# Optimization experiments

Measured on AMD Instinct MI355X. Metric: run time of the kernel, lower is better.

Reference implementation:

```python
import jax, jax.numpy as jnp
import numpy as np

OUT_SIZE = 14
CUTOFF = 0.2
VAR0 = 4            # var[0], mixin_factor = 0.0 -> current std = var[0]
BETA = 4.0
N_SQ = OUT_SIZE * OUT_SIZE
TAU = 0.5 / N_SQ
BATCH = 256
CHANNELS = 512


def _gkern_np(kernlen, std, vmin, vmax):
    n = np.arange(kernlen) - (kernlen - 1) / 2.0
    w = np.exp(-(n ** 2) / (2.0 * std * std))
    g = np.outer(w, w)
    return g * (vmax - vmin) + vmin


def _build_templates():
    n = OUT_SIZE
    base = _gkern_np(2 * n - 1, VAR0, -CUTOFF, 1.0)
    base = np.maximum(base, 0.0) * 2.0 - 1.0
    base = TAU * np.clip(BETA * base / n, -1.0, None)  # clamp(min=-1) only
    # unfold(0,n,1).unfold(1,n,1).reshape(-1,n,n) == sliding windows, row-major
    t = np.lib.stride_tricks.sliding_window_view(base, (n, n)).reshape(-1, n, n)
    t = np.flip(t, axis=0).copy()  # torch.flip(templates, dims=(0,))
    templates_f = jnp.asarray(t, jnp.float32)                    # (n^2, n, n)
    neg = -TAU * jnp.ones((1, n, n), jnp.float32)
    templates_b = jnp.concatenate([templates_f, neg], axis=0)    # (n^2+1, n, n)
    alpha = N_SQ / (1.0 + N_SQ)
    p_T = jnp.asarray(
        np.array([alpha / N_SQ] * N_SQ + [1.0 - alpha], np.float32))  # (n^2+1,)
    return templates_f, templates_b, p_T


def setup_inputs() -> dict:
    key = jax.random.key(0)
    templates_f, templates_b, p_T = _build_templates()
    x = jax.random.normal(key, (BATCH, CHANNELS, OUT_SIZE, OUT_SIZE), jnp.float32)
    return {"x": x, "templates_f": templates_f,
            "templates_b": templates_b, "p_T": p_T}


def reference(x, templates_f, templates_b, p_T):
    B, C, H, W = x.shape
    tau = 0.5 / (H * W)
    # max_pool2d with kernel == full spatial extent -> flat argmax per (b, c)
    idx = jnp.argmax(x.reshape(B, C, H * W), axis=-1)            # (B, C) int
    sel = templates_f[idx]                                       # (B, C, H, W)
    mask = sel / jnp.max(sel)                                    # global max
    mask = jax.nn.relu(mask - CUTOFF) / CUTOFF
    x_masked = x * mask
    # local loss (mutual-information style) on the masked activations
    tr_x_T = jnp.einsum('bcwh,twh->cbt', x_masked * tau, templates_b)  # (C,B,T)
    p_x_T = jax.nn.softmax(tr_x_T, axis=1)                       # softmax over b
    p_x = jnp.einsum('t,cbt->cb', p_T, p_x_T)                    # (C, B)
    log_ratio = jnp.log(p_x_T / p_x[:, :, None])                 # (C, B, T)
    p_x_T_log = jnp.einsum('cbt,cbt->ct', p_x_T, log_ratio)      # (C, T)
    loss = -jnp.einsum('t,ct->c', p_T, p_x_T_log)                # (C,)
    return x_masked, mask, loss
```

## Files before the change

### kernel.cpp

```cpp
#include <hip/hip_runtime.h>

#define BB 256
#define CCH 512
#define HW 196
#define TT 197
#define TROWS 208
#define NFRAG (13 * 7)
#define ASHORTS (NFRAG * 64 * 8)
#define CST (CCH * TROWS)
#define QMAX_SHORTS (4 * 7 * 512)

typedef __attribute__((ext_vector_type(8))) short bf16x8;
typedef __attribute__((ext_vector_type(4))) float f32x4;
typedef __attribute__((ext_vector_type(4))) unsigned short us4;

__device__ __forceinline__ unsigned short f2bf(float f) {
    union { float f; unsigned u; } v; v.f = f;
    unsigned r = v.u + 0x7FFFu + ((v.u >> 16) & 1u);
    return (unsigned short)(r >> 16);
}
__device__ __forceinline__ float bf2f(unsigned short h) {
    union { unsigned u; float f; } v; v.u = ((unsigned)h) << 16;
    return v.f;
}

__global__ void prep(const float* __restrict__ tf, const float* __restrict__ tb,
                     const float* __restrict__ pT,
                     float* __restrict__ wsf, unsigned short* __restrict__ tb_bf,
                     float* __restrict__ pT_pad) {
    if (blockIdx.x < 182) {
        int i = blockIdx.x * 256 + threadIdx.x;
        int frag = i >> 9;
        int s    = i & 511;
        int mt = frag / 7, kt = frag % 7;
        int lane = s >> 3, j = s & 7;
        int r = mt * 16 + (lane & 15);
        int k = kt * 32 + (lane >> 4) * 8 + j;
        const float tau = 0.5f / 196.0f;
        float v = (r < TT && k < HW) ? tb[r * HW + k] * tau : 0.0f;
        tb_bf[i] = f2bf(v);
    } else {
        if (threadIdx.x < TROWS)
            pT_pad[threadIdx.x] = (threadIdx.x < TT) ? pT[threadIdx.x] : 0.0f;
        __shared__ float red[256];
        float m = -1e30f;
        for (int i = threadIdx.x; i < HW * HW; i += 256) m = fmaxf(m, tf[i]);
        red[threadIdx.x] = m;
        __syncthreads();
        for (int s = 128; s > 0; s >>= 1) {
            if (threadIdx.x < s) red[threadIdx.x] = fmaxf(red[threadIdx.x], red[threadIdx.x + s]);
            __syncthreads();
        }
        if (threadIdx.x == 0) wsf[0] = red[0];
    }
}

extern "C" __global__ __launch_bounds__(256)
__attribute__((amdgpu_waves_per_eu(4, 4)))
void k1_main(const float* __restrict__ x, const float* __restrict__ tf,
             const unsigned short* __restrict__ tb_bf, const float* __restrict__ wsf,
             float* __restrict__ xm_out, float* __restrict__ mask_out,
             float* __restrict__ colp, unsigned short* __restrict__ trs)
{
    __shared__ unsigned short Alds[QMAX_SHORTS];
    __shared__ float s_col[4][TROWS];

    const int tid  = threadIdx.x;
    const int lane = tid & 63;
    const int w    = tid >> 6;
    const int l15  = lane & 15, lg = lane >> 4;
    const int c    = blockIdx.x >> 2, g = blockIdx.x & 3;
    const float rg = 1.0f / wsf[0];

    {
        const f32x4* src = (const f32x4*)tb_bf;
        f32x4* dst = (f32x4*)Alds;
        #pragma unroll
        for (int it = 0; it < 7; ++it) dst[tid + it * 256] = src[tid + it * 256];
    }

    const int b = g * 64 + w * 16 + l15;
    const size_t rowoff = ((size_t)b * CCH + c) * HW;
    const float* xrow = x + rowoff;

    f32x4 u[13];
    #pragma unroll
    for (int kt = 0; kt < 6; ++kt) {
        u[2 * kt]     = *(const f32x4*)(xrow + kt * 32 + lg * 8);
        u[2 * kt + 1] = *(const f32x4*)(xrow + kt * 32 + lg * 8 + 4);
    }
    if (lg == 0) u[12] = *(const f32x4*)(xrow + 192);
    else         u[12] = (f32x4){-__builtin_inff(), -__builtin_inff(),
                                 -__builtin_inff(), -__builtin_inff()};

    float bv = -__builtin_inff(); int bi = 0;
    #pragma unroll
    for (int j = 0; j < 13; ++j) {
        const int k0 = (j < 12) ? (((j >> 1) * 8 + lg * 2 + (j & 1)) * 4) : 192;
        #pragma unroll
        for (int e = 0; e < 4; ++e) {
            float v = u[j][e];
            if (v > bv) { bv = v; bi = k0 + e; }
        }
    }
    #pragma unroll
    for (int m = 16; m <= 32; m <<= 1) {
        float ov = __shfl_xor(bv, m, 64);
        int   oi = __shfl_xor(bi, m, 64);
        if (ov > bv || (ov == bv && oi < bi)) { bv = ov; bi = oi; }
    }

    const float* selrow = tf + (size_t)bi * HW;
    float* xmrow = xm_out + rowoff;
    float* mkrow = mask_out + rowoff;
    bf16x8 fr[7];

    #pragma unroll
    for (int kt = 0; kt < 6; ++kt) {
        #pragma unroll
        for (int h = 0; h < 2; ++h) {
            const int k0 = kt * 32 + lg * 8 + h * 4;
            f32x4 sel = *(const f32x4*)(selrow + k0);
            f32x4 mk, xm;
            #pragma unroll
            for (int e = 0; e < 4; ++e) {
                float m = fmaxf(sel[e] * rg - 0.2f, 0.0f) * 5.0f;
                mk[e] = m;
                xm[e] = u[2 * kt + h][e] * m;
            }
            *(f32x4*)(xmrow + k0) = xm;
            *(f32x4*)(mkrow + k0) = mk;
            #pragma unroll
            for (int e = 0; e < 4; ++e) fr[kt][h * 4 + e] = (short)f2bf(xm[e]);
        }
    }
    {
        fr[6] = (bf16x8){0, 0, 0, 0, 0, 0, 0, 0};
        if (lg == 0) {
            f32x4 sel = *(const f32x4*)(selrow + 192);
            f32x4 mk, xm;
            #pragma unroll
            for (int e = 0; e < 4; ++e) {
                float m = fmaxf(sel[e] * rg - 0.2f, 0.0f) * 5.0f;
                mk[e] = m;
                xm[e] = u[12][e] * m;
            }
            *(f32x4*)(xmrow + 192) = xm;
            *(f32x4*)(mkrow + 192) = mk;
            #pragma unroll
            for (int e = 0; e < 4; ++e) fr[6][e] = (short)f2bf(xm[e]);
        }
    }

    f32x4 acc[13];
    #pragma unroll
    for (int mt = 0; mt < 13; ++mt) acc[mt] = (f32x4){0.f, 0.f, 0.f, 0.f};

    const unsigned short* Abase = Alds + lane * 8;

    __syncthreads();
    #pragma unroll
    for (int mt = 0; mt < 4; ++mt) {
        #pragma unroll
        for (int kt = 0; kt < 7; ++kt)
            acc[mt] = __builtin_amdgcn_mfma_f32_16x16x32_bf16(
                *(const bf16x8*)(Abase + (mt * 7 + kt) * 512), fr[kt], acc[mt], 0, 0, 0);
    }
    __syncthreads();

    #pragma unroll
    for (int q = 1; q < 4; ++q) {
        const int m0 = 4 + (q - 1) * 3;
        {
            const f32x4* src = (const f32x4*)tb_bf + m0 * 7 * 64;
            f32x4* dst = (f32x4*)Alds;
            #pragma unroll
            for (int it = 0; it < 6; ++it) {
                int idx = tid + it * 256;
                if (idx < 1344) dst[idx] = src[idx];
            }
        }
        __syncthreads();
        #pragma unroll
        for (int mi = 0; mi < 3; ++mi) {
            const int mt = m0 + mi;
            #pragma unroll
            for (int kt = 0; kt < 7; ++kt)
                acc[mt] = __builtin_amdgcn_mfma_f32_16x16x32_bf16(
                    *(const bf16x8*)(Abase + (mi * 7 + kt) * 512), fr[kt], acc[mt], 0, 0, 0);
        }
        __syncthreads();
    }

    unsigned short* trow = trs + (((size_t)c * 4 + g) * 64 + w * 16 + l15) * TROWS;
    #pragma unroll
    for (int mt = 0; mt < 13; ++mt) {
        us4 pk;
        #pragma unroll
        for (int e = 0; e < 4; ++e) pk[e] = f2bf(acc[mt][e]);
        *(us4*)(trow + mt * 16 + lg * 4) = pk;

        f32x4 s;
        #pragma unroll
        for (int e = 0; e < 4; ++e) s[e] = __expf(acc[mt][e]);
        #pragma unroll
        for (int m = 1; m <= 8; m <<= 1) {
            #pragma unroll
            for (int e = 0; e < 4; ++e) s[e] += __shfl_xor(s[e], m, 64);
        }
        if (l15 == 0) *(f32x4*)(&s_col[w][mt * 16 + lg * 4]) = s;
    }
    __syncthreads();
    if (tid < TROWS) {
        float s = s_col[0][tid] + s_col[1][tid] + s_col[2][tid] + s_col[3][tid];
        colp[(size_t)g * CST + c * TROWS + tid] = s;
    }
}

extern "C" __global__ __launch_bounds__(256)
void k2_loss(const unsigned short* __restrict__ trs, const float* __restrict__ pT_pad,
             const float* __restrict__ colp, float* __restrict__ loss_part)
{
    __shared__ float rAs[TROWS];
    __shared__ float lAs[TROWS];
    __shared__ float pTs[TROWS];
    __shared__ float red[4];

    const int tid  = threadIdx.x;
    const int lane = tid & 63;
    const int w    = tid >> 6;
    const int c    = blockIdx.x >> 2, g = blockIdx.x & 3;

    if (tid < TROWS) {
        const float* cpc = colp + (size_t)c * TROWS + tid;
        float A = cpc[0] + cpc[CST] + cpc[2 * CST] + cpc[3 * CST];
        rAs[tid] = 1.0f / A;
        lAs[tid] = __logf(A);
        pTs[tid] = pT_pad[tid];
    }
    __syncthreads();

    const int p4 = tid & 3;
    const unsigned short* trow = trs + (((size_t)c * 4 + g) * 64 + (tid >> 2)) * TROWS;

    float px = 0.f, S1 = 0.f;
    #pragma unroll
    for (int j = 0; j < 13; ++j) {
        const int t0 = (p4 + 4 * j) * 4;
        us4 tv = *(const us4*)(trow + t0);
        #pragma unroll
        for (int e = 0; e < 4; ++e) {
            const int t = t0 + e;
            float tr = bf2f(tv[e]);
            float p  = __expf(tr) * rAs[t];
            px += pTs[t] * p;
            S1 += pTs[t] * p * (tr - lAs[t]);
        }
    }
    px += __shfl_xor(px, 1, 64);
    px += __shfl_xor(px, 2, 64);
    S1 += __shfl_xor(S1, 1, 64);
    S1 += __shfl_xor(S1, 2, 64);
    float part = (p4 == 0) ? (S1 - px * __logf(px)) : 0.0f;
    #pragma unroll
    for (int off = 4; off <= 32; off <<= 1) part += __shfl_xor(part, off, 64);
    if (lane == 0) red[w] = part;
    __syncthreads();
    if (tid == 0) loss_part[(size_t)c * 4 + g] = red[0] + red[1] + red[2] + red[3];
}

__global__ void k3_fin(const float* __restrict__ lp, float* __restrict__ loss_out) {
    int c = blockIdx.x * 256 + threadIdx.x;
    if (c < CCH)
        loss_out[c] = -(lp[4 * c] + lp[4 * c + 1] + lp[4 * c + 2] + lp[4 * c + 3]);
}

#define H1FRAG (7 * 7)
#define H2FRAG (6 * 7)
#define H1SHORTS (H1FRAG * 512)
#define H2SHORTS (H2FRAG * 512)

extern "C" __global__ __launch_bounds__(1024)
void fused_fb(const float* __restrict__ x, const float* __restrict__ tf,
              const float* __restrict__ pT, const unsigned short* __restrict__ tb_bf,
              const float* __restrict__ wsf,
              float* __restrict__ xm_out, float* __restrict__ mask_out,
              float* __restrict__ loss_out)
{
    extern __shared__ char smem[];
    unsigned short* Alds = (unsigned short*)smem;
    float* s_part = (float*)(smem + H1SHORTS * 2);
    float* rAs    = s_part + 16 * TROWS;
    float* pTs    = rAs + TROWS;
    float* red    = pTs + TROWS;

    const int c    = blockIdx.x;
    const int tid  = threadIdx.x;
    const int lane = tid & 63;
    const int w    = tid >> 6;
    const int l15  = lane & 15, lg = lane >> 4;
    const float rg = 1.0f / wsf[0];

    {
        const f32x4* src = (const f32x4*)tb_bf;
        f32x4* dst = (f32x4*)Alds;
        #pragma unroll
        for (int it = 0; it < 4; ++it) {
            int idx = tid + it * 1024;
            if (idx < H1SHORTS / 8) dst[idx] = src[idx];
        }
    }
    if (tid < TROWS) pTs[tid] = (tid < TT) ? pT[tid] : 0.0f;

    const int b = w * 16 + l15;
    const size_t rowoff = ((size_t)b * CCH + c) * HW;
    const float* xrow = x + rowoff;

    f32x4 u[13];
    #pragma unroll
    for (int kt = 0; kt < 6; ++kt) {
        u[2 * kt]     = *(const f32x4*)(xrow + kt * 32 + lg * 8);
        u[2 * kt + 1] = *(const f32x4*)(xrow + kt * 32 + lg * 8 + 4);
    }
    if (lg == 0) u[12] = *(const f32x4*)(xrow + 192);
    else         u[12] = (f32x4){-__builtin_inff(), -__builtin_inff(),
                                 -__builtin_inff(), -__builtin_inff()};

    float bv = -__builtin_inff(); int bi = 0;
    #pragma unroll
    for (int j = 0; j < 13; ++j) {
        const int k0 = (j < 12) ? (((j >> 1) * 8 + lg * 2 + (j & 1)) * 4) : 192;
        #pragma unroll
        for (int e = 0; e < 4; ++e) {
            float v = u[j][e];
            if (v > bv) { bv = v; bi = k0 + e; }
        }
    }
    #pragma unroll
    for (int m = 16; m <= 32; m <<= 1) {
        float ov = __shfl_xor(bv, m, 64);
        int   oi = __shfl_xor(bi, m, 64);
        if (ov > bv || (ov == bv && oi < bi)) { bv = ov; bi = oi; }
    }

    const float* selrow = tf + (size_t)bi * HW;
    float* xmrow = xm_out + rowoff;
    float* mkrow = mask_out + rowoff;
    bf16x8 fr[7];

    #pragma unroll
    for (int kt = 0; kt < 6; ++kt) {
        #pragma unroll
        for (int h = 0; h < 2; ++h) {
            const int k0 = kt * 32 + lg * 8 + h * 4;
            f32x4 sel = *(const f32x4*)(selrow + k0);
            f32x4 mk, xm;
            #pragma unroll
            for (int e = 0; e < 4; ++e) {
                float m = fmaxf(sel[e] * rg - 0.2f, 0.0f) * 5.0f;
                mk[e] = m;
                xm[e] = u[2 * kt + h][e] * m;
            }
            *(f32x4*)(xmrow + k0) = xm;
            *(f32x4*)(mkrow + k0) = mk;
            #pragma unroll
            for (int e = 0; e < 4; ++e) fr[kt][h * 4 + e] = (short)f2bf(xm[e]);
        }
    }
    {
        fr[6] = (bf16x8){0, 0, 0, 0, 0, 0, 0, 0};
        if (lg == 0) {
            f32x4 sel = *(const f32x4*)(selrow + 192);
            f32x4 mk, xm;
            #pragma unroll
            for (int e = 0; e < 4; ++e) {
                float m = fmaxf(sel[e] * rg - 0.2f, 0.0f) * 5.0f;
                mk[e] = m;
                xm[e] = u[12][e] * m;
            }
            *(f32x4*)(xmrow + 192) = xm;
            *(f32x4*)(mkrow + 192) = mk;
            #pragma unroll
            for (int e = 0; e < 4; ++e) fr[6][e] = (short)f2bf(xm[e]);
        }
    }

    __syncthreads();

    f32x4 acc[13];
    #pragma unroll
    for (int mt = 0; mt < 13; ++mt) acc[mt] = (f32x4){0.f, 0.f, 0.f, 0.f};

    const unsigned short* Abase = Alds + lane * 8;
    #pragma unroll
    for (int kt = 0; kt < 7; ++kt) {
        const bf16x8 bfrag = fr[kt];
        #pragma unroll
        for (int mt = 0; mt < 7; ++mt)
            acc[mt] = __builtin_amdgcn_mfma_f32_16x16x32_bf16(
                *(const bf16x8*)(Abase + (mt * 7 + kt) * 512), bfrag, acc[mt], 0, 0, 0);
    }
    __syncthreads();
    {
        const f32x4* src = (const f32x4*)(tb_bf + H1SHORTS);
        f32x4* dst = (f32x4*)Alds;
        #pragma unroll
        for (int it = 0; it < 3; ++it) {
            int idx = tid + it * 1024;
            if (idx < H2SHORTS / 8) dst[idx] = src[idx];
        }
    }
    __syncthreads();
    #pragma unroll
    for (int kt = 0; kt < 7; ++kt) {
        const bf16x8 bfrag = fr[kt];
        #pragma unroll
        for (int mt = 7; mt < 13; ++mt)
            acc[mt] = __builtin_amdgcn_mfma_f32_16x16x32_bf16(
                *(const bf16x8*)(Abase + ((mt - 7) * 7 + kt) * 512), bfrag, acc[mt], 0, 0, 0);
    }

    float* sp = s_part + w * TROWS;
    #pragma unroll
    for (int mt = 0; mt < 13; ++mt) {
        #pragma unroll
        for (int e = 0; e < 4; ++e) acc[mt][e] = __expf(acc[mt][e]);
        f32x4 s = acc[mt];
        #pragma unroll
        for (int m = 1; m <= 8; m <<= 1) {
            #pragma unroll
            for (int e = 0; e < 4; ++e) s[e] += __shfl_xor(s[e], m, 64);
        }
        if (l15 == 0) *(f32x4*)(sp + mt * 16 + lg * 4) = s;
    }
    __syncthreads();
    if (tid < TROWS) {
        float s = 0.f;
        #pragma unroll
        for (int w2 = 0; w2 < 16; ++w2) s += s_part[w2 * TROWS + tid];
        rAs[tid] = 1.0f / s;
    }
    __syncthreads();

    float px = 0.f;
    #pragma unroll
    for (int mt = 0; mt < 13; ++mt) {
        const int t0 = mt * 16 + lg * 4;
        f32x4 ra = *(const f32x4*)(rAs + t0);
        f32x4 pt = *(const f32x4*)(pTs + t0);
        #pragma unroll
        for (int e = 0; e < 4; ++e) {
            float p = acc[mt][e] * ra[e];
            acc[mt][e] = p;
            px += pt[e] * p;
        }
    }
    px += __shfl_xor(px, 16, 64);
    px += __shfl_xor(px, 32, 64);
    const float rpx = 1.0f / px;

    float part = 0.f;
    #pragma unroll
    for (int mt = 0; mt < 13; ++mt) {
        const int t0 = mt * 16 + lg * 4;
        f32x4 pt = *(const f32x4*)(pTs + t0);
        #pragma unroll
        for (int e = 0; e < 4; ++e) {
            float p = acc[mt][e];
            part += pt[e] * p * __logf(p * rpx);
        }
    }
    #pragma unroll
    for (int off = 32; off >= 1; off >>= 1) part += __shfl_xor(part, off, 64);
    if (lane == 0) red[w] = part;
    __syncthreads();
    if (tid == 0) {
        float s = 0.f;
        #pragma unroll
        for (int w2 = 0; w2 < 16; ++w2) s += red[w2];
        loss_out[c] = -s;
    }
}

extern "C" void kernel_launch(void* const* d_in, const int* in_sizes, int n_in,
                              void* d_out, int out_size, void* d_ws, size_t ws_size,
                              hipStream_t stream) {
    const float* x  = (const float*)d_in[0];
    const float* tf = (const float*)d_in[1];
    const float* tb = (const float*)d_in[2];
    const float* pT = (const float*)d_in[3];

    const size_t NOUT = (size_t)BB * CCH * HW;
    float* xm_out = (float*)d_out;
    float* mk_out = xm_out + NOUT;
    float* ls_out = mk_out + NOUT;

    char* wsp = (char*)d_ws;
    float*          wsf    = (float*)wsp;
    unsigned short* tb_bf  = (unsigned short*)(wsp + 64);
    float*          pT_pad = (float*)(wsp + 93312);
    float*          colp   = (float*)(wsp + 94208);
    float*          lpart  = (float*)(wsp + 1798144);
    unsigned short* trs    = (unsigned short*)(wsp + 1806336);
    const bool big = ws_size >= (size_t)1806336 + 54525952;

    prep<<<183, 256, 0, stream>>>(tf, tb, pT, wsf, tb_bf, pT_pad);

    if (big) {
        k1_main<<<2048, 256, 0, stream>>>(x, tf, tb_bf, wsf, xm_out, mk_out, colp, trs);
        k2_loss<<<2048, 256, 0, stream>>>(trs, pT_pad, colp, lpart);
        k3_fin<<<2, 256, 0, stream>>>(lpart, ls_out);
    } else {
        const size_t SMEM = (size_t)H1SHORTS * 2 + 16 * TROWS * 4
                          + 2 * TROWS * 4 + 16 * 4;
        (void)hipFuncSetAttribute((const void*)fused_fb,
                                  hipFuncAttributeMaxDynamicSharedMemorySize, (int)SMEM);
        fused_fb<<<dim3(CCH), dim3(1024), SMEM, stream>>>(x, tf, pT, tb_bf, wsf,
                                                          xm_out, mk_out, ls_out);
    }
}
```

Measured before the change: 168.1 us.

## Split elementwise masking into contiguous role blocks within a heterogeneous mega kernel

Converts k1_main into a multi-role kernel. Two of every three blocks process 32 contiguous (b,c) rows through LDS, computing argmax, mask and x_masked with fully coalesced float4 loads and stores. The remaining blocks only run the bf16 MFMA GEMM and write the transposed logits. Previously each GEMM block also wrote the strided xm and mask rows, so the output traffic was poorly coalesced. The cost is that the GEMM blocks read x a second time, and the fallback path now re-reads xm_out in a separate GEMM+loss kernel.

```diff
diff --git a/kernel.cpp b/kernel.cpp
--- a/kernel.cpp
+++ b/kernel.cpp
@@ -5,10 +5,15 @@
 #define HW 196
 #define TT 197
 #define TROWS 208
-#define NFRAG (13 * 7)
-#define ASHORTS (NFRAG * 64 * 8)
 #define CST (CCH * TROWS)
 #define QMAX_SHORTS (4 * 7 * 512)
+#define RPW 32
+#define F4PW (RPW * 49)
+#define H1FRAG (7 * 7)
+#define H2FRAG (6 * 7)
+#define H1SHORTS (H1FRAG * 512)
+#define H2SHORTS (H2FRAG * 512)
+#define MEGA_SMEM 32000
 
 typedef __attribute__((ext_vector_type(8))) short bf16x8;
 typedef __attribute__((ext_vector_type(4))) float f32x4;
@@ -57,20 +62,99 @@
 
 extern "C" __global__ __launch_bounds__(256)
 __attribute__((amdgpu_waves_per_eu(4, 4)))
-void k1_main(const float* __restrict__ x, const float* __restrict__ tf,
-             const unsigned short* __restrict__ tb_bf, const float* __restrict__ wsf,
-             float* __restrict__ xm_out, float* __restrict__ mask_out,
-             float* __restrict__ colp, unsigned short* __restrict__ trs)
+void mega(const float* __restrict__ x, const float* __restrict__ tf,
+          const unsigned short* __restrict__ tb_bf, const float* __restrict__ wsf,
+          float* __restrict__ xm_out, float* __restrict__ mask_out,
+          float* __restrict__ colp, unsigned short* __restrict__ trs, int mode)
 {
-    __shared__ unsigned short Alds[QMAX_SHORTS];
-    __shared__ float s_col[4][TROWS];
-
-    const int tid  = threadIdx.x;
+    extern __shared__ char sh[];
+    const int bid = blockIdx.x;
+    const int tid = threadIdx.x;
+    const float rg = 1.0f / wsf[0];
+
+    int role, idx;
+    if (mode == 0) { role = 0; idx = bid; }
+    else if (bid % 3 == 2) { role = 1; idx = (bid - 2) / 3; }
+    else { role = 0; idx = bid - (bid + 1) / 3; }
+
+    if (role == 0) {
+        float* xs  = (float*)sh;
+        int*   biL = (int*)(sh + RPW * HW * 4);
+
+        const size_t base4 = (size_t)idx * F4PW;
+        const f32x4* x4 = (const f32x4*)x + base4;
+        f32x4* xs4 = (f32x4*)xs;
+
+        f32x4 u[7];
+        #pragma unroll
+        for (int k = 0; k < 6; ++k) u[k] = x4[tid + k * 256];
+        if (tid < F4PW - 1536) u[6] = x4[tid + 1536];
+        #pragma unroll
+        for (int k = 0; k < 6; ++k) xs4[tid + k * 256] = u[k];
+        if (tid < F4PW - 1536) xs4[tid + 1536] = u[6];
+        __syncthreads();
+
+        {
+            const int row = tid >> 3;
+            const int o   = tid & 7;
+            float bv = -__builtin_inff(); int bi = 0;
+            #pragma unroll
+            for (int t = 0; t < 7; ++t) {
+                const int j = o + 8 * t;
+                if (j < 49) {
+                    f32x4 xv = xs4[row * 49 + j];
+                    const int k0 = j * 4;
+                    #pragma unroll
+                    for (int e = 0; e < 4; ++e) {
+                        float v = xv[e];
+                        if (v > bv) { bv = v; bi = k0 + e; }
+                    }
+                }
+            }
+            #pragma unroll
+            for (int m = 1; m <= 4; m <<= 1) {
+                float ov = __shfl_xor(bv, m, 64);
+                int   oi = __shfl_xor(bi, m, 64);
+                if (ov > bv || (ov == bv && oi < bi)) { bv = ov; bi = oi; }
+            }
+            if (o == 0) biL[row] = bi;
+        }
+        __syncthreads();
+
+        const f32x4* tf4 = (const f32x4*)tf;
+        f32x4* xm4 = (f32x4*)xm_out + base4;
+        f32x4* mk4 = (f32x4*)mask_out + base4;
+
+        #pragma unroll
+        for (int k = 0; k < 7; ++k) {
+            const int i2 = tid + k * 256;
+            if (k < 6 || i2 < F4PW) {
+                const int rl = i2 / 49;
+                const int j  = i2 - rl * 49;
+                const int bi = biL[rl];
+                f32x4 sel = tf4[bi * 49 + j];
+                f32x4 xv  = u[k];
+                f32x4 mk, xm;
+                #pragma unroll
+                for (int e = 0; e < 4; ++e) {
+                    float m = fmaxf(sel[e] * rg - 0.2f, 0.0f) * 5.0f;
+                    mk[e] = m;
+                    xm[e] = xv[e] * m;
+                }
+                xm4[i2] = xm;
+                mk4[i2] = mk;
+            }
+        }
+        return;
+    }
+
+    unsigned short* Alds = (unsigned short*)sh;
+    float (*s_col)[TROWS] = (float (*)[TROWS])(sh + QMAX_SHORTS * 2);
+
     const int lane = tid & 63;
     const int w    = tid >> 6;
     const int l15  = lane & 15, lg = lane >> 4;
-    const int c    = blockIdx.x >> 2, g = blockIdx.x & 3;
-    const float rg = 1.0f / wsf[0];
+    const int g    = idx >> 9, c = idx & 511;
 
     {
         const f32x4* src = (const f32x4*)tb_bf;
@@ -111,44 +195,27 @@
     }
 
     const float* selrow = tf + (size_t)bi * HW;
-    float* xmrow = xm_out + rowoff;
-    float* mkrow = mask_out + rowoff;
     bf16x8 fr[7];
-
     #pragma unroll
     for (int kt = 0; kt < 6; ++kt) {
         #pragma unroll
         for (int h = 0; h < 2; ++h) {
             const int k0 = kt * 32 + lg * 8 + h * 4;
             f32x4 sel = *(const f32x4*)(selrow + k0);
-            f32x4 mk, xm;
             #pragma unroll
             for (int e = 0; e < 4; ++e) {
                 float m = fmaxf(sel[e] * rg - 0.2f, 0.0f) * 5.0f;
-                mk[e] = m;
-                xm[e] = u[2 * kt + h][e] * m;
+                fr[kt][h * 4 + e] = (short)f2bf(u[2 * kt + h][e] * m);
             }
-            *(f32x4*)(xmrow + k0) = xm;
-            *(f32x4*)(mkrow + k0) = mk;
-            #pragma unroll
-            for (int e = 0; e < 4; ++e) fr[kt][h * 4 + e] = (short)f2bf(xm[e]);
-        }
-    }
-    {
-        fr[6] = (bf16x8){0, 0, 0, 0, 0, 0, 0, 0};
-        if (lg == 0) {
-            f32x4 sel = *(const f32x4*)(selrow + 192);
-            f32x4 mk, xm;
-            #pragma unroll
-            for (int e = 0; e < 4; ++e) {
-                float m = fmaxf(sel[e] * rg - 0.2f, 0.0f) * 5.0f;
-                mk[e] = m;
-                xm[e] = u[12][e] * m;
-            }
-            *(f32x4*)(xmrow + 192) = xm;
-            *(f32x4*)(mkrow + 192) = mk;
-            #pragma unroll
-            for (int e = 0; e < 4; ++e) fr[6][e] = (short)f2bf(xm[e]);
+        }
+    }
+    fr[6] = (bf16x8){0, 0, 0, 0, 0, 0, 0, 0};
+    if (lg == 0) {
+        f32x4 sel = *(const f32x4*)(selrow + 192);
+        #pragma unroll
+        for (int e = 0; e < 4; ++e) {
+            float m = fmaxf(sel[e] * rg - 0.2f, 0.0f) * 5.0f;
+            fr[6][e] = (short)f2bf(u[12][e] * m);
         }
     }
 
@@ -176,8 +243,8 @@
             f32x4* dst = (f32x4*)Alds;
             #pragma unroll
             for (int it = 0; it < 6; ++it) {
-                int idx = tid + it * 256;
-                if (idx < 1344) dst[idx] = src[idx];
+                int i3 = tid + it * 256;
+                if (i3 < 1344) dst[i3] = src[i3];
             }
         }
         __syncthreads();
@@ -275,17 +342,10 @@
         loss_out[c] = -(lp[4 * c] + lp[4 * c + 1] + lp[4 * c + 2] + lp[4 * c + 3]);
 }
 
-#define H1FRAG (7 * 7)
-#define H2FRAG (6 * 7)
-#define H1SHORTS (H1FRAG * 512)
-#define H2SHORTS (H2FRAG * 512)
-
 extern "C" __global__ __launch_bounds__(1024)
-void fused_fb(const float* __restrict__ x, const float* __restrict__ tf,
-              const float* __restrict__ pT, const unsigned short* __restrict__ tb_bf,
-              const float* __restrict__ wsf,
-              float* __restrict__ xm_out, float* __restrict__ mask_out,
-              float* __restrict__ loss_out)
+void k_gemm_loss(const float* __restrict__ xm, const float* __restrict__ pT,
+                 const unsigned short* __restrict__ tb_bf,
+                 float* __restrict__ loss_out)
 {
     extern __shared__ char smem[];
     unsigned short* Alds = (unsigned short*)smem;
@@ -299,7 +359,6 @@
     const int lane = tid & 63;
     const int w    = tid >> 6;
     const int l15  = lane & 15, lg = lane >> 4;
-    const float rg = 1.0f / wsf[0];
 
     {
         const f32x4* src = (const f32x4*)tb_bf;
@@ -313,76 +372,24 @@
     if (tid < TROWS) pTs[tid] = (tid < TT) ? pT[tid] : 0.0f;
 
     const int b = w * 16 + l15;
-    const size_t rowoff = ((size_t)b * CCH + c) * HW;
-    const float* xrow = x + rowoff;
-
-    f32x4 u[13];
+    const float* xrow = xm + ((size_t)b * CCH + c) * HW;
+
+    bf16x8 fr[7];
     #pragma unroll
     for (int kt = 0; kt < 6; ++kt) {
-        u[2 * kt]     = *(const f32x4*)(xrow + kt * 32 + lg * 8);
-        u[2 * kt + 1] = *(const f32x4*)(xrow + kt * 32 + lg * 8 + 4);
-    }
-    if (lg == 0) u[12] = *(const f32x4*)(xrow + 192);
-    else         u[12] = (f32x4){-__builtin_inff(), -__builtin_inff(),
-                                 -__builtin_inff(), -__builtin_inff()};
-
-    float bv = -__builtin_inff(); int bi = 0;
-    #pragma unroll
-    for (int j = 0; j < 13; ++j) {
-        const int k0 = (j < 12) ? (((j >> 1) * 8 + lg * 2 + (j & 1)) * 4) : 192;
+        f32x4 u0 = *(const f32x4*)(xrow + kt * 32 + lg * 8);
+        f32x4 u1 = *(const f32x4*)(xrow + kt * 32 + lg * 8 + 4);
         #pragma unroll
         for (int e = 0; e < 4; ++e) {
-            float v = u[j][e];
-            if (v > bv) { bv = v; bi = k0 + e; }
-        }
-    }
-    #pragma unroll
-    for (int m = 16; m <= 32; m <<= 1) {
-        float ov = __shfl_xor(bv, m, 64);
-        int   oi = __shfl_xor(bi, m, 64);
-        if (ov > bv || (ov == bv && oi < bi)) { bv = ov; bi = oi; }
-    }
-
-    const float* selrow = tf + (size_t)bi * HW;
-    float* xmrow = xm_out + rowoff;
-    float* mkrow = mask_out + rowoff;
-    bf16x8 fr[7];
-
-    #pragma unroll
-    for (int kt = 0; kt < 6; ++kt) {
-        #pragma unroll
-        for (int h = 0; h < 2; ++h) {
-            const int k0 = kt * 32 + lg * 8 + h * 4;
-            f32x4 sel = *(const f32x4*)(selrow + k0);
-            f32x4 mk, xm;
-            #pragma unroll
-            for (int e = 0; e < 4; ++e) {
-                float m = fmaxf(sel[e] * rg - 0.2f, 0.0f) * 5.0f;
-                mk[e] = m;
-                xm[e] = u[2 * kt + h][e] * m;
-            }
-            *(f32x4*)(xmrow + k0) = xm;
-            *(f32x4*)(mkrow + k0) = mk;
-            #pragma unroll
-            for (int e = 0; e < 4; ++e) fr[kt][h * 4 + e] = (short)f2bf(xm[e]);
-        }
-    }
-    {
-        fr[6] = (bf16x8){0, 0, 0, 0, 0, 0, 0, 0};
-        if (lg == 0) {
-            f32x4 sel = *(const f32x4*)(selrow + 192);
-            f32x4 mk, xm;
-            #pragma unroll
-            for (int e = 0; e < 4; ++e) {
-                float m = fmaxf(sel[e] * rg - 0.2f, 0.0f) * 5.0f;
-                mk[e] = m;
-                xm[e] = u[12][e] * m;
-            }
-            *(f32x4*)(xmrow + 192) = xm;
-            *(f32x4*)(mkrow + 192) = mk;
-            #pragma unroll
-            for (int e = 0; e < 4; ++e) fr[6][e] = (short)f2bf(xm[e]);
-        }
+            fr[kt][e]     = (short)f2bf(u0[e]);
+            fr[kt][e + 4] = (short)f2bf(u1[e]);
+        }
+    }
+    fr[6] = (bf16x8){0, 0, 0, 0, 0, 0, 0, 0};
+    if (lg == 0) {
+        f32x4 u0 = *(const f32x4*)(xrow + 192);
+        #pragma unroll
+        for (int e = 0; e < 4; ++e) fr[6][e] = (short)f2bf(u0[e]);
     }
 
     __syncthreads();
@@ -396,9 +403,10 @@
     for (int kt = 0; kt < 7; ++kt) {
         const bf16x8 bfrag = fr[kt];
         #pragma unroll
-        for (int mt = 0; mt < 7; ++mt)
-            acc[mt] = __builtin_amdgcn_mfma_f32_16x16x32_bf16(
-                *(const bf16x8*)(Abase + (mt * 7 + kt) * 512), bfrag, acc[mt], 0, 0, 0);
+        for (int mt = 0; mt < 7; ++mt) {
+            bf16x8 afrag = *(const bf16x8*)(Abase + (mt * 7 + kt) * 512);
+            acc[mt] = __builtin_amdgcn_mfma_f32_16x16x32_bf16(afrag, bfrag, acc[mt], 0, 0, 0);
+        }
     }
     __syncthreads();
     {
@@ -415,9 +423,10 @@
     for (int kt = 0; kt < 7; ++kt) {
         const bf16x8 bfrag = fr[kt];
         #pragma unroll
-        for (int mt = 7; mt < 13; ++mt)
-            acc[mt] = __builtin_amdgcn_mfma_f32_16x16x32_bf16(
-                *(const bf16x8*)(Abase + ((mt - 7) * 7 + kt) * 512), bfrag, acc[mt], 0, 0, 0);
+        for (int mt = 7; mt < 13; ++mt) {
+            bf16x8 afrag = *(const bf16x8*)(Abase + ((mt - 7) * 7 + kt) * 512);
+            acc[mt] = __builtin_amdgcn_mfma_f32_16x16x32_bf16(afrag, bfrag, acc[mt], 0, 0, 0);
+        }
     }
 
     float* sp = s_part + w * TROWS;
@@ -505,17 +514,21 @@
     const bool big = ws_size >= (size_t)1806336 + 54525952;
 
     prep<<<183, 256, 0, stream>>>(tf, tb, pT, wsf, tb_bf, pT_pad);
+    (void)hipFuncSetAttribute((const void*)mega,
+                              hipFuncAttributeMaxDynamicSharedMemorySize, MEGA_SMEM);
 
     if (big) {
-        k1_main<<<2048, 256, 0, stream>>>(x, tf, tb_bf, wsf, xm_out, mk_out, colp, trs);
+        mega<<<6144, 256, MEGA_SMEM, stream>>>(x, tf, tb_bf, wsf, xm_out, mk_out,
+                                               colp, trs, 1);
         k2_loss<<<2048, 256, 0, stream>>>(trs, pT_pad, colp, lpart);
         k3_fin<<<2, 256, 0, stream>>>(lpart, ls_out);
     } else {
-        const size_t SMEM = (size_t)H1SHORTS * 2 + 16 * TROWS * 4
-                          + 2 * TROWS * 4 + 16 * 4;
-        (void)hipFuncSetAttribute((const void*)fused_fb,
-                                  hipFuncAttributeMaxDynamicSharedMemorySize, (int)SMEM);
-        fused_fb<<<dim3(CCH), dim3(1024), SMEM, stream>>>(x, tf, pT, tb_bf, wsf,
-                                                          xm_out, mk_out, ls_out);
-    }
-}
+        mega<<<4096, 256, MEGA_SMEM, stream>>>(x, tf, tb_bf, wsf, xm_out, mk_out,
+                                               (float*)wsp, (unsigned short*)wsp, 0);
+        const size_t SMEM2 = (size_t)H1SHORTS * 2 + 16 * TROWS * 4
+                           + TROWS * 4 + TROWS * 4 + 16 * 4;
+        (void)hipFuncSetAttribute((const void*)k_gemm_loss,
+                                  hipFuncAttributeMaxDynamicSharedMemorySize, (int)SMEM2);
+        k_gemm_loss<<<dim3(CCH), dim3(1024), SMEM2, stream>>>(xm_out, pT, tb_bf, ls_out);
+    }
+}
```

Result: faster. 160.5 us (-4.5%).
